# Kernel optimization log

Hardware: AMD Instinct MI355X
Metric: run time of the kernel (lower is better)

## Reference

```python
import jax, jax.numpy as jnp
import numpy as np

B, N, C = 128, 8732, 21  # batch, SSD priors, VOC classes (incl. background)
EPS = 1e-7


def setup_inputs() -> dict:
    key = jax.random.key(0)
    k1, k2, k3 = jax.random.split(key, 3)
    return {
        "lam": jnp.float32(0.7),
        "conf": jax.random.uniform(k1, (B, N, C), dtype=jnp.float32),
        "conf_shuffle": jax.random.uniform(k2, (B, N, C), dtype=jnp.float32),
        "conf_interpolation": jax.random.uniform(k3, (B, N, C), dtype=jnp.float32),
    }


def reference(lam, conf, conf_shuffle, conf_interpolation):
    half = conf.shape[0] // 2
    # swap the two halves of the shuffled batch
    conf_temp = jnp.concatenate([conf_shuffle[half:], conf_shuffle[:half]], axis=0)

    # foreground mask: max class score beats background score, on both sides
    left_mask = jnp.max(conf[..., 1:], axis=-1) > conf[..., 0]
    right_mask = jnp.max(conf_temp[..., 1:], axis=-1) > conf_temp[..., 0]
    mask = (left_mask & right_mask).astype(conf.dtype)  # [B, N]

    mixed = lam * conf + (1.0 - lam) * conf_temp + EPS
    inter = conf_interpolation + EPS

    sg = jax.lax.stop_gradient
    # KLDivLoss(log_input, target) = target * (log(target) - log_input), summed over classes
    inter_t = sg(inter)
    kl_a = jnp.sum(inter_t * (jnp.log(inter_t) - jnp.log(mixed)), axis=-1)  # [B, N]
    mixed_t = sg(mixed)
    kl_b = jnp.sum(mixed_t * (jnp.log(mixed_t) - jnp.log(inter)), axis=-1)  # [B, N]

    cnt = jnp.sum(mask)
    # masked mean over selected (b, n) samples; 0 if mask empty
    loss = jnp.sum((kl_a + kl_b) * mask) / jnp.maximum(cnt, 1.0)
    return jnp.where(cnt > 0, loss / 2.0, jnp.float32(0.0))
```

## Files before the change

kernel.cpp:

```cpp
#include <hip/hip_runtime.h>


#define EPS 1e-7f

constexpr int B = 128;
constexpr int N = 8732;
constexpr int C = 21;
constexpr int ROWS = B * N;
constexpr int TILE = 256;
constexpr int BLOCK = 256;
constexpr int GRID = ROWS / TILE;
constexpr int TILE_ELEMS = TILE * C;
constexpr int TILE_F4 = TILE_ELEMS / 4;
constexpr int BATCH_F4 = (N * C) / 4;

__global__ __launch_bounds__(BLOCK) void isd_main_kernel(
    const float* __restrict__ lam_p,
    const float* __restrict__ conf,
    const float* __restrict__ csh,
    const float* __restrict__ cin,
    double* __restrict__ partials)
{
    __shared__ float s_conf[TILE_ELEMS];
    __shared__ float s_csh [TILE_ELEMS];
    __shared__ float s_cin [TILE_ELEMS];

    const int tid = threadIdx.x;
    const int tileF4base = blockIdx.x * TILE_F4;

    const float4* conf4 = (const float4*)conf;
    const float4* csh4  = (const float4*)csh;
    const float4* cin4  = (const float4*)cin;

    for (int k = tid; k < TILE_F4; k += BLOCK) {
        const int G = tileF4base + k;
        ((float4*)s_conf)[k] = conf4[G];
        ((float4*)s_cin )[k] = cin4[G];
        const int b  = G / BATCH_F4;
        const int G2 = G + ((b ^ 64) - b) * BATCH_F4;
        ((float4*)s_csh)[k] = csh4[G2];
    }
    __syncthreads();

    const float lam = lam_p[0];
    const float oml = 1.0f - lam;

    const float* pc = s_conf + tid * C;
    const float* pt = s_csh  + tid * C;
    const float* pi = s_cin  + tid * C;

    float c0 = 0.0f, t0 = 0.0f;
    float cmax = -1e30f, tmax = -1e30f;
    float kl = 0.0f;

    #pragma unroll
    for (int c = 0; c < C; ++c) {
        const float cv = pc[c];
        const float tv = pt[c];
        const float iv = pi[c] + EPS;
        const float mv = fmaf(lam, cv, oml * tv) + EPS;
        kl += (iv - mv) * (__logf(iv) - __logf(mv));
        if (c == 0) { c0 = cv; t0 = tv; }
        else        { cmax = fmaxf(cmax, cv); tmax = fmaxf(tmax, tv); }
    }

    const float msk = ((cmax > c0) && (tmax > t0)) ? 1.0f : 0.0f;
    float sum = kl * msk;
    float cnt = msk;

    #pragma unroll
    for (int off = 32; off > 0; off >>= 1) {
        sum += __shfl_down(sum, off, 64);
        cnt += __shfl_down(cnt, off, 64);
    }

    __shared__ float r_sum[BLOCK / 64];
    __shared__ float r_cnt[BLOCK / 64];
    const int wave = tid >> 6;
    const int lane = tid & 63;
    if (lane == 0) { r_sum[wave] = sum; r_cnt[wave] = cnt; }
    __syncthreads();

    if (tid == 0) {
        double bs = 0.0, bc = 0.0;
        #pragma unroll
        for (int w = 0; w < BLOCK / 64; ++w) { bs += (double)r_sum[w]; bc += (double)r_cnt[w]; }
        partials[2 * blockIdx.x + 0] = bs;
        partials[2 * blockIdx.x + 1] = bc;
    }
}

__global__ __launch_bounds__(256) void isd_final_kernel(
    const double* __restrict__ partials,
    float* __restrict__ out)
{
    double s = 0.0, c = 0.0;
    for (int i = threadIdx.x; i < GRID; i += 256) {
        s += partials[2 * i + 0];
        c += partials[2 * i + 1];
    }
    #pragma unroll
    for (int off = 32; off > 0; off >>= 1) {
        s += __shfl_down(s, off, 64);
        c += __shfl_down(c, off, 64);
    }
    __shared__ double ss[4], sc[4];
    const int wave = threadIdx.x >> 6;
    const int lane = threadIdx.x & 63;
    if (lane == 0) { ss[wave] = s; sc[wave] = c; }
    __syncthreads();
    if (threadIdx.x == 0) {
        const double S  = ss[0] + ss[1] + ss[2] + ss[3];
        const double Cc = sc[0] + sc[1] + sc[2] + sc[3];
        out[0] = (Cc > 0.0) ? (float)(S / fmax(Cc, 1.0) * 0.5) : 0.0f;
    }
}

extern "C" void kernel_launch(void* const* d_in, const int* in_sizes, int n_in,
                              void* d_out, int out_size, void* d_ws, size_t ws_size,
                              hipStream_t stream) {
    const float* lam  = (const float*)d_in[0];
    const float* conf = (const float*)d_in[1];
    const float* csh  = (const float*)d_in[2];
    const float* cin  = (const float*)d_in[3];
    float* out = (float*)d_out;
    double* partials = (double*)d_ws;

    isd_main_kernel<<<GRID, BLOCK, 0, stream>>>(lam, conf, csh, cin, partials);
    isd_final_kernel<<<1, 256, 0, stream>>>(partials, out);
}
```

Before: 274.7 us.

## Replace LDS tile staging with direct per-thread float4 loads over 4-row groups

Drops the shared-memory staging of conf, shuffled conf and interpolation tiles. Each thread now handles a group of 4 consecutive rows (84 floats, 21 float4) and loads them straight from global memory with float4 reads into registers. This removes LDS traffic, bank conflicts on the stride-21 reads and the block barrier, and cuts the grid by 4x. In exchange, each thread's loads are strided across lanes (84 floats apart), which hurts coalescing, and register pressure rises.

```diff
diff --git a/kernel.cpp b/kernel.cpp
--- a/kernel.cpp
+++ b/kernel.cpp
@@ -7,11 +7,10 @@
 constexpr int N = 8732;
 constexpr int C = 21;
 constexpr int ROWS = B * N;
-constexpr int TILE = 256;
+constexpr int GROUPS = ROWS / 4;
 constexpr int BLOCK = 256;
-constexpr int GRID = ROWS / TILE;
-constexpr int TILE_ELEMS = TILE * C;
-constexpr int TILE_F4 = TILE_ELEMS / 4;
+constexpr int GRID = (GROUPS + BLOCK - 1) / BLOCK;
+constexpr int NB4 = N / 4;
 constexpr int BATCH_F4 = (N * C) / 4;
 
 __global__ __launch_bounds__(BLOCK) void isd_main_kernel(
@@ -21,52 +20,64 @@
     const float* __restrict__ cin,
     double* __restrict__ partials)
 {
-    __shared__ float s_conf[TILE_ELEMS];
-    __shared__ float s_csh [TILE_ELEMS];
-    __shared__ float s_cin [TILE_ELEMS];
-
-    const int tid = threadIdx.x;
-    const int tileF4base = blockIdx.x * TILE_F4;
+    const float lam = lam_p[0];
+    const float oml = 1.0f - lam;
 
     const float4* conf4 = (const float4*)conf;
     const float4* csh4  = (const float4*)csh;
     const float4* cin4  = (const float4*)cin;
 
-    for (int k = tid; k < TILE_F4; k += BLOCK) {
-        const int G = tileF4base + k;
-        ((float4*)s_conf)[k] = conf4[G];
-        ((float4*)s_cin )[k] = cin4[G];
-        const int b  = G / BATCH_F4;
-        const int G2 = G + ((b ^ 64) - b) * BATCH_F4;
-        ((float4*)s_csh)[k] = csh4[G2];
+    const int t = blockIdx.x * BLOCK + threadIdx.x;
+
+    float sum = 0.0f;
+    float cnt = 0.0f;
+
+    if (t < GROUPS) {
+        const int b  = t / NB4;
+        const int g  = t - b * NB4;
+        const size_t f4c = (size_t)t * 21;
+        const size_t f4s = (size_t)(b ^ 64) * BATCH_F4 + (size_t)g * 21;
+
+        #pragma unroll
+        for (int j = 0; j < 4; ++j) {
+            const int fs = (21 * j) >> 2;
+
+            float4 ax[6], sx[6], ix[6];
+            #pragma unroll
+            for (int q = 0; q < 6; ++q) {
+                ax[q] = conf4[f4c + fs + q];
+                sx[q] = csh4 [f4s + fs + q];
+                ix[q] = cin4 [f4c + fs + q];
+            }
+
+            float av[24], sv[24], iv_[24];
+            #pragma unroll
+            for (int q = 0; q < 6; ++q) {
+                av[4*q+0] = ax[q].x; av[4*q+1] = ax[q].y; av[4*q+2] = ax[q].z; av[4*q+3] = ax[q].w;
+                sv[4*q+0] = sx[q].x; sv[4*q+1] = sx[q].y; sv[4*q+2] = sx[q].z; sv[4*q+3] = sx[q].w;
+                iv_[4*q+0] = ix[q].x; iv_[4*q+1] = ix[q].y; iv_[4*q+2] = ix[q].z; iv_[4*q+3] = ix[q].w;
+            }
+
+            float c0 = 0.0f, t0 = 0.0f;
+            float cmax = -1e30f, tmax = -1e30f;
+            float kl = 0.0f;
+
+            #pragma unroll
+            for (int c = 0; c < C; ++c) {
+                const float cv = av[j + c];
+                const float tv = sv[j + c];
+                const float iv = iv_[j + c] + EPS;
+                const float mv = fmaf(lam, cv, oml * tv) + EPS;
+                kl += (iv - mv) * (__logf(iv) - __logf(mv));
+                if (c == 0) { c0 = cv; t0 = tv; }
+                else        { cmax = fmaxf(cmax, cv); tmax = fmaxf(tmax, tv); }
+            }
+
+            const float msk = ((cmax > c0) && (tmax > t0)) ? 1.0f : 0.0f;
+            sum += kl * msk;
+            cnt += msk;
+        }
     }
-    __syncthreads();
-
-    const float lam = lam_p[0];
-    const float oml = 1.0f - lam;
-
-    const float* pc = s_conf + tid * C;
-    const float* pt = s_csh  + tid * C;
-    const float* pi = s_cin  + tid * C;
-
-    float c0 = 0.0f, t0 = 0.0f;
-    float cmax = -1e30f, tmax = -1e30f;
-    float kl = 0.0f;
-
-    #pragma unroll
-    for (int c = 0; c < C; ++c) {
-        const float cv = pc[c];
-        const float tv = pt[c];
-        const float iv = pi[c] + EPS;
-        const float mv = fmaf(lam, cv, oml * tv) + EPS;
-        kl += (iv - mv) * (__logf(iv) - __logf(mv));
-        if (c == 0) { c0 = cv; t0 = tv; }
-        else        { cmax = fmaxf(cmax, cv); tmax = fmaxf(tmax, tv); }
-    }
-
-    const float msk = ((cmax > c0) && (tmax > t0)) ? 1.0f : 0.0f;
-    float sum = kl * msk;
-    float cnt = msk;
 
     #pragma unroll
     for (int off = 32; off > 0; off >>= 1) {
@@ -76,12 +87,12 @@
 
     __shared__ float r_sum[BLOCK / 64];
     __shared__ float r_cnt[BLOCK / 64];
-    const int wave = tid >> 6;
-    const int lane = tid & 63;
+    const int wave = threadIdx.x >> 6;
+    const int lane = threadIdx.x & 63;
     if (lane == 0) { r_sum[wave] = sum; r_cnt[wave] = cnt; }
     __syncthreads();
 
-    if (tid == 0) {
+    if (threadIdx.x == 0) {
         double bs = 0.0, bc = 0.0;
         #pragma unroll
         for (int w = 0; w < BLOCK / 64; ++w) { bs += (double)r_sum[w]; bc += (double)r_cnt[w]; }
```

After: 374.3 us. 1.36x slower.
